# Performance work log

Measured on AMD Instinct MI355X. Metric: run time of the kernel, lower is better.

The kernel has to match this reference:

```python
import jax, jax.numpy as jnp
import numpy as np

B = 2
ROW, COL = 63, 84          # resolution
ROW_, COL_ = 32, 42        # resolution_
N = ROW * COL              # 5292 kv tokens
N_ = ROW_ * COL_           # 1344 q tokens
IN_DIM, OUT_DIM = 256, 512
KEY_DIM, NUM_HEADS, ATTN_RATIO, STRIDE = 16, 8, 2, 2
D = ATTN_RATIO * KEY_DIM   # 32 (value dim per head)
DH = D * NUM_HEADS         # 256
NH_KD = KEY_DIM * NUM_HEADS  # 128
H_KV = DH + NH_KD          # 384
SCALE = KEY_DIM ** -0.5
EPS = 1e-5


def _build_bias_idxs():
    # replicates the itertools.product double loop, vectorized; ids ordered by
    # first occurrence in row-major scan (same as dict insertion order).
    r_ = np.arange(ROW_); c_ = np.arange(COL_)
    r = np.arange(ROW); c = np.arange(COL)
    off_r = np.abs(r_[:, None] * STRIDE - r[None, :])      # (32, 63)
    off_c = np.abs(c_[:, None] * STRIDE - c[None, :])      # (42, 84)
    keys = (off_r[:, None, :, None] * 1000 + off_c[None, :, None, :]).reshape(-1)
    _, first_idx, inv = np.unique(keys, return_index=True, return_inverse=True)
    order = np.argsort(first_idx)
    rank = np.empty_like(order); rank[order] = np.arange(len(order))
    idxs = rank[inv].reshape(N_, N).astype(np.int32)
    return idxs, len(order)


def setup_inputs() -> dict:
    key = jax.random.key(0)
    ks = jax.random.split(key, 12)
    idxs_np, n_off = _build_bias_idxs()
    inp = {
        "x": jax.random.normal(ks[0], (B, N, IN_DIM), jnp.float32),
        "kv_w": jax.random.normal(ks[1], (H_KV, IN_DIM), jnp.float32) * (IN_DIM ** -0.5),
        "kv_g": jnp.ones((H_KV,), jnp.float32),
        "kv_b": jnp.zeros((H_KV,), jnp.float32),
        "q_w": jax.random.normal(ks[2], (NH_KD, IN_DIM), jnp.float32) * (IN_DIM ** -0.5),
        "q_g": jnp.ones((NH_KD,), jnp.float32),
        "q_b": jnp.zeros((NH_KD,), jnp.float32),
        "proj_w": jax.random.normal(ks[3], (OUT_DIM, DH), jnp.float32) * (DH ** -0.5),
        "proj_g": jnp.ones((OUT_DIM,), jnp.float32),
        "proj_b": jnp.zeros((OUT_DIM,), jnp.float32),
        "bias_table": jax.random.normal(ks[4], (NUM_HEADS, n_off), jnp.float32) * 0.02,
        "bias_idxs": jnp.asarray(idxs_np),
    }
    return inp


def _linear_bn(x, w, g, b):
    # Linear (no bias) followed by BatchNorm1d in training mode (batch stats
    # over flattened (B*N) dim, biased variance).
    y = jnp.einsum("bnc,oc->bno", x, w)
    flat = y.reshape(-1, y.shape[-1])
    mu = flat.mean(0)
    var = flat.var(0)
    return (y - mu) * (g / jnp.sqrt(var + EPS)) + b


def _hardswish(x):
    return x * jnp.clip(x + 3.0, 0.0, 6.0) / 6.0


def reference(x, kv_w, kv_g, kv_b, q_w, q_g, q_b, proj_w, proj_g, proj_b,
              bias_table, bias_idxs):
    Bx = x.shape[0]
    # kv projection -> split k (KEY_DIM) and v (D) per head
    kv = _linear_bn(x, kv_w, kv_g, kv_b).reshape(Bx, N, NUM_HEADS, KEY_DIM + D)
    k = kv[..., :KEY_DIM].transpose(0, 2, 1, 3)   # (B, H, N, key_dim)
    v = kv[..., KEY_DIM:].transpose(0, 2, 1, 3)   # (B, H, N, d)
    # q: spatial subsample then projection
    xs = x.reshape(Bx, ROW, COL, IN_DIM)[:, ::STRIDE, ::STRIDE].reshape(Bx, N_, IN_DIM)
    q = _linear_bn(xs, q_w, q_g, q_b).reshape(Bx, N_, NUM_HEADS, KEY_DIM).transpose(0, 2, 1, 3)
    # gathered relative position bias: (H, N_, N)
    ab = bias_table[:, bias_idxs]
    attn = jnp.einsum("bhqd,bhkd->bhqk", q, k) * SCALE + ab[None]
    attn = jax.nn.softmax(attn, axis=-1)
    out = jnp.einsum("bhqk,bhkd->bhqd", attn, v)       # (B, H, N_, d)
    out = out.transpose(0, 2, 1, 3).reshape(Bx, N_, DH)
    out = _linear_bn(_hardswish(out), proj_w, proj_g, proj_b)
    return out
```

## Files before the change

### kernel.cpp

```cpp
#include <hip/hip_runtime.h>
#include <hip/hip_bf16.h>
#include <math.h>

#define N_K 5292
#define N_Q 1344
#define NH_KD 128
#define NROWS 21504
#define LOG2E 1.4426950408889634f
#define MSTAT 16.0f

typedef float f32x4 __attribute__((ext_vector_type(4)));
typedef short short8 __attribute__((ext_vector_type(8)));

__device__ __forceinline__ float fexp2(float x) {
#if __has_builtin(__builtin_amdgcn_exp2f)
    return __builtin_amdgcn_exp2f(x);
#else
    return exp2f(x);
#endif
}

__device__ __forceinline__ unsigned pk_bf16(float a, float b) {
    union { __hip_bfloat162 h; unsigned u; } c;
    c.h = __float22bfloat162_rn(make_float2(a, b));
    return c.u;
}

__device__ __forceinline__ void hilo_pk(float4 v, uint2& hi, uint2& lo) {
    unsigned h0 = pk_bf16(v.x, v.y);
    unsigned h1 = pk_bf16(v.z, v.w);
    float hx = __uint_as_float(h0 << 16);
    float hy = __uint_as_float(h0 & 0xffff0000u);
    float hz = __uint_as_float(h1 << 16);
    float hw = __uint_as_float(h1 & 0xffff0000u);
    hi = make_uint2(h0, h1);
    lo = make_uint2(pk_bf16(v.x - hx, v.y - hy), pk_bf16(v.z - hz, v.w - hw));
}

__global__ __launch_bounds__(256) void prep_kernel(
    const float* __restrict__ x, const float* __restrict__ kv_w,
    const float* __restrict__ q_w, const float* __restrict__ proj_w,
    const float* __restrict__ bias_table, const int* __restrict__ bias_idxs, int n_off,
    float* __restrict__ sums, unsigned short* __restrict__ Xh, unsigned short* __restrict__ Xl,
    unsigned short* __restrict__ Wh, unsigned short* __restrict__ Wl,
    float* __restrict__ bt_r)
{
    int bid = blockIdx.x;
    const int t = threadIdx.x;
    if (bid < 8) {
        int i = bid * 256 + t;
        if (i < 2048) sums[i] = 0.f;
        return;
    }
    bid -= 8;
    if (bid < 2646) {
        int i = bid * 256 + t;
        float4 v = ((const float4*)x)[i];
        uint2 h, l;
        hilo_pk(v, h, l);
        ((uint2*)Xh)[i] = h;
        ((uint2*)Xl)[i] = l;
        return;
    }
    bid -= 2646;
    if (bid < 256) {
        int i = bid * 256 + t;
        int j = i;
        const float* s;
        if (j < 384 * 64) s = kv_w;
        else if ((j -= 384 * 64) < 128 * 64) s = q_w;
        else { j -= 128 * 64; s = proj_w; }
        float4 v = ((const float4*)s)[j];
        uint2 h, l;
        hilo_pk(v, h, l);
        ((uint2*)Wh)[i] = h;
        ((uint2*)Wl)[i] = l;
        return;
    }
    bid -= 256;
    {
        int i = bid * 256 + t;
        if (i < 8 * N_K) {
            int h = i / N_K, j = i - h * N_K;
            bt_r[i] = fmaf(bias_table[h * n_off + bias_idxs[j]], LOG2E, -MSTAT);
        }
    }
}

__device__ __forceinline__ void gemm_core(
    const unsigned short* __restrict__ Ah, const unsigned short* __restrict__ Al,
    const unsigned short* __restrict__ Wh, const unsigned short* __restrict__ Wl,
    float* __restrict__ Y, float* __restrict__ sums,
    int M, int Ncols, int mtiles, int nblk, int mode, int id)
{
    __shared__ unsigned short As_h[64][40], As_l[64][40], Bs_h[64][40], Bs_l[64][40];
    const int xcd = id & 7;
    const int id8 = id >> 3;
    const int my = xcd + (id8 / nblk) * 8;
    const int ny = id8 % nblk;
    if (my >= mtiles) return;

    const int t = threadIdx.x;
    const int w = t >> 6, lane = t & 63, g = lane >> 4, ln = lane & 15;
    const int m0 = my * 64, n0 = ny * 64;
    const int srow = t >> 2;
    const int sc8 = (t & 3) * 8;

    int mrow = m0 + srow;
    long asrc = -1;
    if (mrow < M) {
        if (mode == 1) {
            int bb = mrow / N_Q;
            int i = mrow - bb * N_Q;
            asrc = (long)(bb * N_K + (i / 42) * 168 + (i % 42) * 2);
        } else asrc = mrow;
    }
    const int nrow = n0 + srow;

    f32x4 acc[4];
    #pragma unroll
    for (int nt = 0; nt < 4; ++nt) acc[nt] = (f32x4){0.f, 0.f, 0.f, 0.f};

    for (int k0 = 0; k0 < 256; k0 += 32) {
        uint4 a_h = make_uint4(0, 0, 0, 0), a_l = a_h;
        if (asrc >= 0) {
            a_h = *(const uint4*)(Ah + asrc * 256 + k0 + sc8);
            a_l = *(const uint4*)(Al + asrc * 256 + k0 + sc8);
        }
        uint4 b_h = *(const uint4*)(Wh + (size_t)nrow * 256 + k0 + sc8);
        uint4 b_l = *(const uint4*)(Wl + (size_t)nrow * 256 + k0 + sc8);

        __syncthreads();
        *(uint4*)&As_h[srow][sc8] = a_h;
        *(uint4*)&As_l[srow][sc8] = a_l;
        *(uint4*)&Bs_h[srow][sc8] = b_h;
        *(uint4*)&Bs_l[srow][sc8] = b_l;
        __syncthreads();

        short8 ah = *(const short8*)&As_h[w * 16 + ln][g * 8];
        short8 al = *(const short8*)&As_l[w * 16 + ln][g * 8];
        #pragma unroll
        for (int nt = 0; nt < 4; ++nt) {
            short8 bh = *(const short8*)&Bs_h[nt * 16 + ln][g * 8];
            short8 bl = *(const short8*)&Bs_l[nt * 16 + ln][g * 8];
            acc[nt] = __builtin_amdgcn_mfma_f32_16x16x32_bf16(al, bh, acc[nt], 0, 0, 0);
            acc[nt] = __builtin_amdgcn_mfma_f32_16x16x32_bf16(ah, bl, acc[nt], 0, 0, 0);
            acc[nt] = __builtin_amdgcn_mfma_f32_16x16x32_bf16(ah, bh, acc[nt], 0, 0, 0);
        }
    }

    #pragma unroll
    for (int nt = 0; nt < 4; ++nt) {
        #pragma unroll
        for (int reg = 0; reg < 4; ++reg) {
            int mr = m0 + w * 16 + g * 4 + reg;
            if (mr < M) Y[(size_t)mr * Ncols + n0 + nt * 16 + ln] = acc[nt][reg];
        }
    }

    float s4[4], q4[4];
    #pragma unroll
    for (int nt = 0; nt < 4; ++nt) {
        float s = acc[nt][0] + acc[nt][1] + acc[nt][2] + acc[nt][3];
        float q = fmaf(acc[nt][0], acc[nt][0], fmaf(acc[nt][1], acc[nt][1],
                  fmaf(acc[nt][2], acc[nt][2], acc[nt][3] * acc[nt][3])));
        s += __shfl_xor(s, 16); s += __shfl_xor(s, 32);
        q += __shfl_xor(q, 16); q += __shfl_xor(q, 32);
        s4[nt] = s; q4[nt] = q;
    }
    __syncthreads();
    float* st_s = (float*)&As_h[0][0];
    float* st_q = st_s + 256;
    if (g == 0) {
        #pragma unroll
        for (int nt = 0; nt < 4; ++nt) {
            st_s[(w * 4 + nt) * 16 + ln] = s4[nt];
            st_q[(w * 4 + nt) * 16 + ln] = q4[nt];
        }
    }
    __syncthreads();
    if (t < 64) {
        int nt = t >> 4, c = t & 15;
        float a = 0.f, b2 = 0.f;
        #pragma unroll
        for (int ww = 0; ww < 4; ++ww) {
            a  += st_s[(ww * 4 + nt) * 16 + c];
            b2 += st_q[(ww * 4 + nt) * 16 + c];
        }
        atomicAdd(&sums[n0 + nt * 16 + c], a);
        atomicAdd(&sums[Ncols + n0 + nt * 16 + c], b2);
    }
}

__global__ __launch_bounds__(256) void gemm_qkv(
    const unsigned short* __restrict__ Xh, const unsigned short* __restrict__ Xl,
    const unsigned short* __restrict__ Wh, const unsigned short* __restrict__ Wl,
    float* __restrict__ kv_y, float* __restrict__ q_y,
    float* __restrict__ sums_kv, float* __restrict__ sums_q)
{
    int id = blockIdx.x;
    if (id < 1008)
        gemm_core(Xh, Xl, Wh, Wl, kv_y, sums_kv, 10584, 384, 166, 6, 0, id);
    else
        gemm_core(Xh, Xl, Wh + 384 * 256, Wl + 384 * 256, q_y, sums_q,
                  2688, 128, 42, 2, 1, id - 1008);
}

__global__ __launch_bounds__(256) void gemm_proj(
    const unsigned short* __restrict__ Ah, const unsigned short* __restrict__ Al,
    const unsigned short* __restrict__ Wh, const unsigned short* __restrict__ Wl,
    float* __restrict__ Y, float* __restrict__ sums)
{
    gemm_core(Ah, Al, Wh, Wl, Y, sums, 2688, 512, 42, 8, 0, blockIdx.x);
}

__global__ __launch_bounds__(256) void kv_pack(const float* __restrict__ kv_y,
                                               const float* __restrict__ sums,
                                               const float* __restrict__ kv_g,
                                               const float* __restrict__ kv_b,
                                               unsigned short* __restrict__ Kp,
                                               unsigned short* __restrict__ Vp)
{
    int i = blockIdx.x * 256 + threadIdx.x;
    if (i >= 2 * 8 * N_K * 12) return;
    int c4 = i % 12;
    int key = (i / 12) % N_K;
    int h = (i / (12 * N_K)) & 7;
    int b = i / (12 * N_K * 8);
    int ch = h * 48 + c4 * 4;
    const float inv = 1.f / 10584.f;
    float4 sm = *(const float4*)(sums + ch);
    float4 sq = *(const float4*)(sums + 384 + ch);
    float4 gg = *(const float4*)(kv_g + ch);
    float4 bb = *(const float4*)(kv_b + ch);
    float4 v = *(const float4*)(kv_y + (size_t)(b * N_K + key) * 384 + ch);
    #define BNAPP(c) { float mu = sm.c * inv; \
        float var = fmaf(-mu, mu, sq.c * inv); \
        float s = gg.c * rsqrtf(var + 1e-5f); \
        v.c = fmaf(v.c, s, fmaf(-mu, s, bb.c)); }
    BNAPP(x) BNAPP(y) BNAPP(z) BNAPP(w)
    #undef BNAPP
    uint2 u = make_uint2(pk_bf16(v.x, v.y), pk_bf16(v.z, v.w));
    size_t slot = (size_t)(b * 8 + h) * N_K + key;
    if (c4 < 4) *(uint2*)((unsigned*)Kp + slot * 8 + c4 * 2) = u;
    else        *(uint2*)((unsigned*)Vp + slot * 16 + (c4 - 4) * 2) = u;
}

__global__ __launch_bounds__(256, 5) void attn_mfma(
    const unsigned short* __restrict__ Kp, const unsigned short* __restrict__ Vp,
    const float* __restrict__ q_y, const float* __restrict__ sums,
    const float* __restrict__ q_g, const float* __restrict__ q_b,
    const float* __restrict__ bt_r,
    float* __restrict__ pl, float* __restrict__ pacc)
{
    const int id = blockIdx.x;
    const int h = id & 7;
    const int z = (id >> 3) & 7;
    const int qt = id >> 6;
    const int b = z >> 2, ks = z & 3;
    const int t = threadIdx.x;
    const int w = t >> 6, lane = t & 63, g = lane >> 4, ln = lane & 15;

    __shared__ float bt_s[21 * 84];
    __shared__ unsigned short K_s[2][64][24];
    __shared__ unsigned short Vt_s[2][32][72];
    __shared__ unsigned short P_s[4][16][72];

    const int q0 = qt * 64;
    const int kstart = ks * 1344;
    const int kend = (kstart + 1344 < N_K) ? kstart + 1344 : N_K;
    const int ntiles = (kend - kstart + 63) >> 6;
    const bool tail = (ks == 3);

    const int kr0 = ks * 16;
    const int kr1 = (kend - 1) / 84;
    const int rq2min = (q0 / 42) * 2;
    const int rq2max = ((q0 + 63) / 42) * 2;
    int dr_lo = 0;
    if (rq2min > kr1) dr_lo = rq2min - kr1;
    else if (kr0 > rq2max) dr_lo = kr0 - rq2max;
    int a1 = rq2max - kr0, a2 = kr1 - rq2min;
    int dr_hi = a1 > a2 ? a1 : a2;
    {
        int nb = (dr_hi - dr_lo + 1) * 84;
        const float* src = bt_r + h * N_K + dr_lo * 84;
        for (int j = t; j < nb; j += 256) bt_s[j] = src[j];
    }

    short8 qfrag = (short8)0;
    if (lane < 32) {
        const float inv = 1.f / 2688.f;
        const float post = 0.25f * LOG2E;
        const int c0 = h * 16 + g * 8;
        const float* qp = q_y + (size_t)(b * N_Q + q0 + w * 16 + ln) * NH_KD + c0;
        float vv[8];
        #pragma unroll
        for (int j = 0; j < 8; ++j) {
            float mu  = sums[c0 + j] * inv;
            float var = fmaf(-mu, mu, sums[128 + c0 + j] * inv);
            float s   = q_g[c0 + j] * rsqrtf(var + 1e-5f) * post;
            vv[j] = fmaf(qp[j], s, fmaf(-mu, s, q_b[c0 + j] * post));
        }
        union { short8 s; unsigned u[4]; } qf;
        qf.u[0] = pk_bf16(vv[0], vv[1]); qf.u[1] = pk_bf16(vv[2], vv[3]);
        qf.u[2] = pk_bf16(vv[4], vv[5]); qf.u[3] = pk_bf16(vv[6], vv[7]);
        qfrag = qf.s;
    }

    int rq2[4], cq2[4];
    #pragma unroll
    for (int reg = 0; reg < 4; ++reg) {
        int qg = q0 + w * 16 + g * 4 + reg;
        rq2[reg] = (qg / 42) * 2;
        cq2[reg] = (qg % 42) * 2;
    }
    int kr[4], kc[4];
    #pragma unroll
    for (int st = 0; st < 4; ++st) {
        int kg = kstart + st * 16 + ln;
        kr[st] = kg / 84;
        kc[st] = kg - kr[st] * 84;
    }

    const unsigned* kp_base = (const unsigned*)Kp + (size_t)(b * 8 + h) * N_K * 8;
    const unsigned* vp_base = (const unsigned*)Vp + (size_t)(b * 8 + h) * N_K * 16;
    const int skey = t >> 2, schunk = t & 3;
    const int vslot = ((skey & 15) << 2) | (skey >> 4);
    const int v0 = schunk * 8;

    uint2 kreg; uint4 vreg;
    {
        int kg = kstart + skey; if (kg > N_K - 1) kg = N_K - 1;
        kreg = *(const uint2*)(kp_base + (size_t)kg * 8 + schunk * 2);
        vreg = *(const uint4*)(vp_base + (size_t)kg * 16 + schunk * 4);
    }
    *(uint2*)&K_s[0][skey][schunk * 4] = kreg;
    Vt_s[0][v0 + 0][vslot] = (unsigned short)vreg.x;
    Vt_s[0][v0 + 1][vslot] = (unsigned short)(vreg.x >> 16);
    Vt_s[0][v0 + 2][vslot] = (unsigned short)vreg.y;
    Vt_s[0][v0 + 3][vslot] = (unsigned short)(vreg.y >> 16);
    Vt_s[0][v0 + 4][vslot] = (unsigned short)vreg.z;
    Vt_s[0][v0 + 5][vslot] = (unsigned short)(vreg.z >> 16);
    Vt_s[0][v0 + 6][vslot] = (unsigned short)vreg.w;
    Vt_s[0][v0 + 7][vslot] = (unsigned short)(vreg.w >> 16);
    __syncthreads();

    float l[4] = {0.f, 0.f, 0.f, 0.f};
    f32x4 acc0 = {0.f, 0.f, 0.f, 0.f}, acc1 = {0.f, 0.f, 0.f, 0.f};
    const f32x4 zero4 = {0.f, 0.f, 0.f, 0.f};
    int p = 0;

    for (int it = 0; it < ntiles; ++it) {
        const int k0 = kstart + it * 64;
        const bool notlast = (it + 1 < ntiles);
        if (notlast) {
            int kg = k0 + 64 + skey; if (kg > N_K - 1) kg = N_K - 1;
            kreg = *(const uint2*)(kp_base + (size_t)kg * 8 + schunk * 2);
            vreg = *(const uint4*)(vp_base + (size_t)kg * 16 + schunk * 4);
        }

        f32x4 sf[4];
        #pragma unroll
        for (int st = 0; st < 4; ++st) {
            short8 bf = (short8)0;
            if (lane < 32) bf = *(const short8*)&K_s[p][st * 16 + ln][g * 8];
            sf[st] = __builtin_amdgcn_mfma_f32_16x16x32_bf16(qfrag, bf, zero4, 0, 0, 0);
        }

        float pv[4][4];
        #pragma unroll
        for (int st = 0; st < 4; ++st) {
            #pragma unroll
            for (int reg = 0; reg < 4; ++reg) {
                int dr = rq2[reg] - kr[st]; dr = dr < 0 ? -dr : dr;
                int dc = cq2[reg] - kc[st]; dc = dc < 0 ? -dc : dc;
                pv[st][reg] = fexp2(sf[st][reg] + bt_s[(dr - dr_lo) * 84 + dc]);
            }
        }
        if (tail && it == ntiles - 1) {
            #pragma unroll
            for (int st = 0; st < 4; ++st) {
                bool bad = (k0 + st * 16 + ln) >= N_K;
                #pragma unroll
                for (int reg = 0; reg < 4; ++reg)
                    pv[st][reg] = bad ? 0.f : pv[st][reg];
            }
        }

        #pragma unroll
        for (int reg = 0; reg < 4; ++reg) {
            l[reg] += (pv[0][reg] + pv[1][reg]) + (pv[2][reg] + pv[3][reg]);
            uint2 pw = make_uint2(pk_bf16(pv[0][reg], pv[1][reg]),
                                  pk_bf16(pv[2][reg], pv[3][reg]));
            *(uint2*)&P_s[w][g * 4 + reg][4 * ln] = pw;
        }

        #pragma unroll
        for (int kt = 0; kt < 2; ++kt) {
            short8 af = *(const short8*)&P_s[w][ln][g * 8 + kt * 32];
            short8 b0 = *(const short8*)&Vt_s[p][ln][g * 8 + kt * 32];
            short8 b1 = *(const short8*)&Vt_s[p][ln + 16][g * 8 + kt * 32];
            acc0 = __builtin_amdgcn_mfma_f32_16x16x32_bf16(af, b0, acc0, 0, 0, 0);
            acc1 = __builtin_amdgcn_mfma_f32_16x16x32_bf16(af, b1, acc1, 0, 0, 0);
        }

        if (notlast) {
            int q2 = p ^ 1;
            *(uint2*)&K_s[q2][skey][schunk * 4] = kreg;
            Vt_s[q2][v0 + 0][vslot] = (unsigned short)vreg.x;
            Vt_s[q2][v0 + 1][vslot] = (unsigned short)(vreg.x >> 16);
            Vt_s[q2][v0 + 2][vslot] = (unsigned short)vreg.y;
            Vt_s[q2][v0 + 3][vslot] = (unsigned short)(vreg.y >> 16);
            Vt_s[q2][v0 + 4][vslot] = (unsigned short)vreg.z;
            Vt_s[q2][v0 + 5][vslot] = (unsigned short)(vreg.z >> 16);
            Vt_s[q2][v0 + 6][vslot] = (unsigned short)vreg.w;
            Vt_s[q2][v0 + 7][vslot] = (unsigned short)(vreg.w >> 16);
            __syncthreads();
            p = q2;
        }

        #pragma unroll
        for (int st = 0; st < 4; ++st) {
            kc[st] += 64;
            if (kc[st] >= 84) { kc[st] -= 84; kr[st] += 1; }
        }
    }

    #pragma unroll
    for (int reg = 0; reg < 4; ++reg) {
        float s = l[reg];
        s += __shfl_xor(s, 1, 16);
        s += __shfl_xor(s, 2, 16);
        s += __shfl_xor(s, 4, 16);
        s += __shfl_xor(s, 8, 16);
        l[reg] = s;
    }

    const int rbase = (b * 8 + h) * N_Q + q0 + w * 16;
    #pragma unroll
    for (int reg = 0; reg < 4; ++reg) {
        int prow = ks * NROWS + rbase + g * 4 + reg;
        pacc[(size_t)prow * 32 + ln]      = acc0[reg];
        pacc[(size_t)prow * 32 + 16 + ln] = acc1[reg];
        if (ln == 0) pl[prow] = l[reg];
    }
}

__global__ __launch_bounds__(256) void combine_kernel(const float* __restrict__ pl,
                                                      const float* __restrict__ pacc,
                                                      unsigned short* __restrict__ oh,
                                                      unsigned short* __restrict__ ol)
{
    int i = blockIdx.x * 256 + threadIdx.x;
    int r = i >> 5, e = i & 31;
    float L = (pl[r] + pl[NROWS + r]) + (pl[2 * NROWS + r] + pl[3 * NROWS + r]);
    float v = (pacc[(size_t)r * 32 + e] + pacc[(size_t)(NROWS + r) * 32 + e])
            + (pacc[(size_t)(2 * NROWS + r) * 32 + e] + pacc[(size_t)(3 * NROWS + r) * 32 + e]);
    v /= L;
    float hs = v * fminf(fmaxf(v + 3.f, 0.f), 6.f) * (1.f / 6.f);
    unsigned hu = pk_bf16(hs, 0.f) & 0xffffu;
    float hf = __uint_as_float(hu << 16);
    unsigned lu = pk_bf16(hs - hf, 0.f) & 0xffffu;
    int q = r % N_Q;
    int bh = r / N_Q;
    int hh = bh & 7, b = bh >> 3;
    size_t idx = (size_t)(b * N_Q + q) * 256 + hh * 32 + e;
    oh[idx] = (unsigned short)hu;
    ol[idx] = (unsigned short)lu;
}

__global__ __launch_bounds__(256) void norm_apply(
    const float* __restrict__ Y, const float* __restrict__ sums,
    const float* __restrict__ g, const float* __restrict__ bb,
    float* __restrict__ out, int rows, int cols, float inv_rows)
{
    __shared__ float sc_s[64], sh_s[64];
    const int t = threadIdx.x;
    const int c0 = blockIdx.x * 64;
    if (t < 64) {
        int c = c0 + t;
        float mu  = sums[c] * inv_rows;
        float var = fmaf(-mu, mu, sums[cols + c] * inv_rows);
        float s   = g[c] * rsqrtf(var + 1e-5f);
        sc_s[t] = s;
        sh_s[t] = fmaf(-mu, s, bb[c]);
    }
    __syncthreads();
    const int c4 = (t & 15) * 4;
    float4 scv = *(const float4*)&sc_s[c4];
    float4 shv = *(const float4*)&sh_s[c4];
    for (int r = blockIdx.y * 16 + (t >> 4); r < rows; r += gridDim.y * 16) {
        size_t off = (size_t)r * cols + c0 + c4;
        float4 v = *(const float4*)(Y + off);
        v.x = fmaf(v.x, scv.x, shv.x);
        v.y = fmaf(v.y, scv.y, shv.y);
        v.z = fmaf(v.z, scv.z, shv.z);
        v.w = fmaf(v.w, scv.w, shv.w);
        *(float4*)(out + off) = v;
    }
}

extern "C" void kernel_launch(void* const* d_in, const int* in_sizes, int n_in,
                              void* d_out, int out_size, void* d_ws, size_t ws_size,
                              hipStream_t stream) {
    (void)n_in; (void)out_size; (void)ws_size;
    const float* x      = (const float*)d_in[0];
    const float* kv_w   = (const float*)d_in[1];
    const float* kv_g   = (const float*)d_in[2];
    const float* kv_b   = (const float*)d_in[3];
    const float* q_w    = (const float*)d_in[4];
    const float* q_g    = (const float*)d_in[5];
    const float* q_b    = (const float*)d_in[6];
    const float* proj_w = (const float*)d_in[7];
    const float* proj_g = (const float*)d_in[8];
    const float* proj_b = (const float*)d_in[9];
    const float* bias_table = (const float*)d_in[10];
    const int*   bias_idxs  = (const int*)d_in[11];
    const int    n_off = in_sizes[10] / 8;
    float* out = (float*)d_out;

    float* ws = (float*)d_ws;
    float* kv_y = ws;
    float* q_y  = kv_y + 10584 * 384;
    float* regA = q_y + 2688 * 128;
    unsigned short* Xh = (unsigned short*)regA;
    unsigned short* Xl = Xh + 10584 * 256;
    float* pacc   = regA;
    float* proj_y = regA;
    float* pl = regA + 4 * NROWS * 32;
    unsigned short* Wh = (unsigned short*)(pl + 4 * NROWS);
    unsigned short* Wl = Wh + 1024 * 256;
    unsigned short* attn_oh = Wl + 1024 * 256;
    unsigned short* attn_ol = attn_oh + 2688 * 256;
    unsigned short* Kp = attn_ol + 2688 * 256;
    unsigned short* Vp = Kp + 2 * 8 * N_K * 16;
    float* sums_kv = (float*)(Vp + 2 * 8 * N_K * 32);
    float* sums_q  = sums_kv + 768;
    float* sums_p  = sums_q + 256;
    float* bt_r    = sums_p + 1024;

    prep_kernel<<<3076, 256, 0, stream>>>(x, kv_w, q_w, proj_w, bias_table, bias_idxs,
                                          n_off, sums_kv, Xh, Xl, Wh, Wl, bt_r);
    gemm_qkv<<<1104, 256, 0, stream>>>(Xh, Xl, Wh, Wl, kv_y, q_y, sums_kv, sums_q);
    kv_pack<<<3969, 256, 0, stream>>>(kv_y, sums_kv, kv_g, kv_b, Kp, Vp);
    attn_mfma<<<1344, 256, 0, stream>>>(Kp, Vp, q_y, sums_q, q_g, q_b, bt_r, pl, pacc);
    combine_kernel<<<2688, 256, 0, stream>>>(pl, pacc, attn_oh, attn_ol);
    gemm_proj<<<384, 256, 0, stream>>>(attn_oh, attn_ol, Wh + 512 * 256, Wl + 512 * 256,
                                       proj_y, sums_p);
    norm_apply<<<dim3(8, 84), 256, 0, stream>>>(proj_y, sums_p, proj_g, proj_b, out,
                                                2688, 512, 1.f / 2688.f);
}
```

Measured before the change: 222.1 us.

## Drop split-bf16 GEMM precision and fold kv BatchNorm into attention and combine

The GEMMs now run in plain bf16 instead of the hi/lo three-MFMA split, which cuts MFMA work and operand traffic to a third. The kv GEMM writes raw bf16 K and V directly in the packed per-head layout, so the kv_pack kernel and the fp32 kv_y buffer go away. The kv BatchNorm is applied algebraically instead: the K scale is folded into q, the K shift is dropped because it is constant along each softmax row, and the V affine is applied in combine. This loses precision, since raw K and V are rounded to bf16 before normalisation and no low-order correction is kept, and it may break tolerance.

```diff
diff --git a/kernel.cpp b/kernel.cpp
--- a/kernel.cpp
+++ b/kernel.cpp
@@ -25,25 +25,16 @@
     c.h = __float22bfloat162_rn(make_float2(a, b));
     return c.u;
 }
-
-__device__ __forceinline__ void hilo_pk(float4 v, uint2& hi, uint2& lo) {
-    unsigned h0 = pk_bf16(v.x, v.y);
-    unsigned h1 = pk_bf16(v.z, v.w);
-    float hx = __uint_as_float(h0 << 16);
-    float hy = __uint_as_float(h0 & 0xffff0000u);
-    float hz = __uint_as_float(h1 << 16);
-    float hw = __uint_as_float(h1 & 0xffff0000u);
-    hi = make_uint2(h0, h1);
-    lo = make_uint2(pk_bf16(v.x - hx, v.y - hy), pk_bf16(v.z - hz, v.w - hw));
+__device__ __forceinline__ unsigned short f2bf(float a) {
+    return (unsigned short)pk_bf16(a, 0.f);
 }
 
 __global__ __launch_bounds__(256) void prep_kernel(
     const float* __restrict__ x, const float* __restrict__ kv_w,
     const float* __restrict__ q_w, const float* __restrict__ proj_w,
     const float* __restrict__ bias_table, const int* __restrict__ bias_idxs, int n_off,
-    float* __restrict__ sums, unsigned short* __restrict__ Xh, unsigned short* __restrict__ Xl,
-    unsigned short* __restrict__ Wh, unsigned short* __restrict__ Wl,
-    float* __restrict__ bt_r)
+    float* __restrict__ sums, unsigned short* __restrict__ Xp,
+    unsigned short* __restrict__ Wp, float* __restrict__ bt_r)
 {
     int bid = blockIdx.x;
     const int t = threadIdx.x;
@@ -56,10 +47,7 @@
     if (bid < 2646) {
         int i = bid * 256 + t;
         float4 v = ((const float4*)x)[i];
-        uint2 h, l;
-        hilo_pk(v, h, l);
-        ((uint2*)Xh)[i] = h;
-        ((uint2*)Xl)[i] = l;
+        ((uint2*)Xp)[i] = make_uint2(pk_bf16(v.x, v.y), pk_bf16(v.z, v.w));
         return;
     }
     bid -= 2646;
@@ -71,10 +59,7 @@
         else if ((j -= 384 * 64) < 128 * 64) s = q_w;
         else { j -= 128 * 64; s = proj_w; }
         float4 v = ((const float4*)s)[j];
-        uint2 h, l;
-        hilo_pk(v, h, l);
-        ((uint2*)Wh)[i] = h;
-        ((uint2*)Wl)[i] = l;
+        ((uint2*)Wp)[i] = make_uint2(pk_bf16(v.x, v.y), pk_bf16(v.z, v.w));
         return;
     }
     bid -= 256;
@@ -87,77 +72,40 @@
     }
 }
 
-__device__ __forceinline__ void gemm_core(
-    const unsigned short* __restrict__ Ah, const unsigned short* __restrict__ Al,
-    const unsigned short* __restrict__ Wh, const unsigned short* __restrict__ Wl,
-    float* __restrict__ Y, float* __restrict__ sums,
-    int M, int Ncols, int mtiles, int nblk, int mode, int id)
-{
-    __shared__ unsigned short As_h[64][40], As_l[64][40], Bs_h[64][40], Bs_l[64][40];
-    const int xcd = id & 7;
-    const int id8 = id >> 3;
-    const int my = xcd + (id8 / nblk) * 8;
-    const int ny = id8 % nblk;
-    if (my >= mtiles) return;
-
+__device__ __forceinline__ void gemm_body(
+    const unsigned short* __restrict__ Ap, const unsigned short* __restrict__ Wp,
+    long asrc, int nrow,
+    unsigned short (*As)[40], unsigned short (*Bs)[40], f32x4 acc[4])
+{
     const int t = threadIdx.x;
     const int w = t >> 6, lane = t & 63, g = lane >> 4, ln = lane & 15;
-    const int m0 = my * 64, n0 = ny * 64;
     const int srow = t >> 2;
     const int sc8 = (t & 3) * 8;
 
-    int mrow = m0 + srow;
-    long asrc = -1;
-    if (mrow < M) {
-        if (mode == 1) {
-            int bb = mrow / N_Q;
-            int i = mrow - bb * N_Q;
-            asrc = (long)(bb * N_K + (i / 42) * 168 + (i % 42) * 2);
-        } else asrc = mrow;
-    }
-    const int nrow = n0 + srow;
-
-    f32x4 acc[4];
-    #pragma unroll
-    for (int nt = 0; nt < 4; ++nt) acc[nt] = (f32x4){0.f, 0.f, 0.f, 0.f};
-
     for (int k0 = 0; k0 < 256; k0 += 32) {
-        uint4 a_h = make_uint4(0, 0, 0, 0), a_l = a_h;
-        if (asrc >= 0) {
-            a_h = *(const uint4*)(Ah + asrc * 256 + k0 + sc8);
-            a_l = *(const uint4*)(Al + asrc * 256 + k0 + sc8);
-        }
-        uint4 b_h = *(const uint4*)(Wh + (size_t)nrow * 256 + k0 + sc8);
-        uint4 b_l = *(const uint4*)(Wl + (size_t)nrow * 256 + k0 + sc8);
+        uint4 a = make_uint4(0, 0, 0, 0);
+        if (asrc >= 0) a = *(const uint4*)(Ap + asrc * 256 + k0 + sc8);
+        uint4 b = *(const uint4*)(Wp + (size_t)nrow * 256 + k0 + sc8);
 
         __syncthreads();
-        *(uint4*)&As_h[srow][sc8] = a_h;
-        *(uint4*)&As_l[srow][sc8] = a_l;
-        *(uint4*)&Bs_h[srow][sc8] = b_h;
-        *(uint4*)&Bs_l[srow][sc8] = b_l;
+        *(uint4*)&As[srow][sc8] = a;
+        *(uint4*)&Bs[srow][sc8] = b;
         __syncthreads();
 
-        short8 ah = *(const short8*)&As_h[w * 16 + ln][g * 8];
-        short8 al = *(const short8*)&As_l[w * 16 + ln][g * 8];
+        short8 ah = *(const short8*)&As[w * 16 + ln][g * 8];
         #pragma unroll
         for (int nt = 0; nt < 4; ++nt) {
-            short8 bh = *(const short8*)&Bs_h[nt * 16 + ln][g * 8];
-            short8 bl = *(const short8*)&Bs_l[nt * 16 + ln][g * 8];
-            acc[nt] = __builtin_amdgcn_mfma_f32_16x16x32_bf16(al, bh, acc[nt], 0, 0, 0);
-            acc[nt] = __builtin_amdgcn_mfma_f32_16x16x32_bf16(ah, bl, acc[nt], 0, 0, 0);
+            short8 bh = *(const short8*)&Bs[nt * 16 + ln][g * 8];
             acc[nt] = __builtin_amdgcn_mfma_f32_16x16x32_bf16(ah, bh, acc[nt], 0, 0, 0);
         }
     }
-
-    #pragma unroll
-    for (int nt = 0; nt < 4; ++nt) {
-        #pragma unroll
-        for (int reg = 0; reg < 4; ++reg) {
-            int mr = m0 + w * 16 + g * 4 + reg;
-            if (mr < M) Y[(size_t)mr * Ncols + n0 + nt * 16 + ln] = acc[nt][reg];
-        }
-    }
-
+}
+
+__device__ __forceinline__ void gemm_stats(f32x4 acc[4], float* __restrict__ sums,
+                                           int n0, int Ncols, float* scratch)
+{
+    const int t = threadIdx.x;
+    const int w = t >> 6, lane = t & 63, g = lane >> 4, ln = lane & 15;
     float s4[4], q4[4];
     #pragma unroll
     for (int nt = 0; nt < 4; ++nt) {
@@ -169,8 +117,8 @@
         s4[nt] = s; q4[nt] = q;
     }
     __syncthreads();
-    float* st_s = (float*)&As_h[0][0];
-    float* st_q = st_s + 256;
+    float* st_s = scratch;
+    float* st_q = scratch + 256;
     if (g == 0) {
         #pragma unroll
         for (int nt = 0; nt < 4; ++nt) {
@@ -193,63 +141,106 @@
 }
 
 __global__ __launch_bounds__(256) void gemm_qkv(
-    const unsigned short* __restrict__ Xh, const unsigned short* __restrict__ Xl,
-    const unsigned short* __restrict__ Wh, const unsigned short* __restrict__ Wl,
-    float* __restrict__ kv_y, float* __restrict__ q_y,
-    float* __restrict__ sums_kv, float* __restrict__ sums_q)
-{
+    const unsigned short* __restrict__ Xp, const unsigned short* __restrict__ Wp,
+    unsigned short* __restrict__ Kp, unsigned short* __restrict__ Vp,
+    float* __restrict__ q_y, float* __restrict__ sums_kv, float* __restrict__ sums_q)
+{
+    __shared__ unsigned short As[64][40], Bs[64][40];
+    const int t = threadIdx.x;
+    const int w = t >> 6, lane = t & 63, g = lane >> 4, ln = lane & 15;
+    const int srow = t >> 2;
     int id = blockIdx.x;
-    if (id < 1008)
-        gemm_core(Xh, Xl, Wh, Wl, kv_y, sums_kv, 10584, 384, 166, 6, 0, id);
-    else
-        gemm_core(Xh, Xl, Wh + 384 * 256, Wl + 384 * 256, q_y, sums_q,
-                  2688, 128, 42, 2, 1, id - 1008);
+
+    f32x4 acc[4];
+    #pragma unroll
+    for (int nt = 0; nt < 4; ++nt) acc[nt] = (f32x4){0.f, 0.f, 0.f, 0.f};
+
+    if (id < 1008) {
+        const int xcd = id & 7, id8 = id >> 3;
+        const int my = xcd + (id8 / 6) * 8, ny = id8 % 6;
+        if (my >= 166) return;
+        const int m0 = my * 64, n0 = ny * 64;
+        int mrow = m0 + srow;
+        long asrc = (mrow < 10584) ? mrow : -1;
+        gemm_body(Xp, Wp, asrc, n0 + srow, As, Bs, acc);
+
+        #pragma unroll
+        for (int nt = 0; nt < 4; ++nt) {
+            int c = n0 + nt * 16 + ln;
+            int hh = c / 48, cc = c - 48 * hh;
+            #pragma unroll
+            for (int reg = 0; reg < 4; ++reg) {
+                int mr = m0 + w * 16 + g * 4 + reg;
+                if (mr < 10584) {
+                    int bb = mr >= N_K;
+                    int key = mr - bb * N_K;
+                    unsigned short v16 = f2bf(acc[nt][reg]);
+                    size_t slot = (size_t)(bb * 8 + hh) * N_K + key;
+                    if (cc < 16) Kp[slot * 16 + cc] = v16;
+                    else         Vp[slot * 32 + cc - 16] = v16;
+                }
+            }
+        }
+        gemm_stats(acc, sums_kv, n0, 384, (float*)&As[0][0]);
+    } else {
+        id -= 1008;
+        const int xcd = id & 7, id8 = id >> 3;
+        const int my = xcd + (id8 / 2) * 8, ny = id8 % 2;
+        if (my >= 42) return;
+        const int m0 = my * 64, n0 = ny * 64;
+        int mrow = m0 + srow;
+        long asrc = -1;
+        {
+            int bb = mrow / N_Q;
+            int i = mrow - bb * N_Q;
+            asrc = (long)(bb * N_K + (i / 42) * 168 + (i % 42) * 2);
+        }
+        gemm_body(Xp, Wp + 384 * 256, asrc, n0 + srow, As, Bs, acc);
+
+        #pragma unroll
+        for (int nt = 0; nt < 4; ++nt)
+            #pragma unroll
+            for (int reg = 0; reg < 4; ++reg) {
+                int mr = m0 + w * 16 + g * 4 + reg;
+                q_y[(size_t)mr * 128 + n0 + nt * 16 + ln] = acc[nt][reg];
+            }
+        gemm_stats(acc, sums_q, n0, 128, (float*)&As[0][0]);
+    }
 }
 
 __global__ __launch_bounds__(256) void gemm_proj(
-    const unsigned short* __restrict__ Ah, const unsigned short* __restrict__ Al,
-    const unsigned short* __restrict__ Wh, const unsigned short* __restrict__ Wl,
+    const unsigned short* __restrict__ Ap, const unsigned short* __restrict__ Wp,
     float* __restrict__ Y, float* __restrict__ sums)
 {
-    gemm_core(Ah, Al, Wh, Wl, Y, sums, 2688, 512, 42, 8, 0, blockIdx.x);
-}
-
-__global__ __launch_bounds__(256) void kv_pack(const float* __restrict__ kv_y,
-                                               const float* __restrict__ sums,
-                                               const float* __restrict__ kv_g,
-                                               const float* __restrict__ kv_b,
-                                               unsigned short* __restrict__ Kp,
-                                               unsigned short* __restrict__ Vp)
-{
-    int i = blockIdx.x * 256 + threadIdx.x;
-    if (i >= 2 * 8 * N_K * 12) return;
-    int c4 = i % 12;
-    int key = (i / 12) % N_K;
-    int h = (i / (12 * N_K)) & 7;
-    int b = i / (12 * N_K * 8);
-    int ch = h * 48 + c4 * 4;
-    const float inv = 1.f / 10584.f;
-    float4 sm = *(const float4*)(sums + ch);
-    float4 sq = *(const float4*)(sums + 384 + ch);
-    float4 gg = *(const float4*)(kv_g + ch);
-    float4 bb = *(const float4*)(kv_b + ch);
-    float4 v = *(const float4*)(kv_y + (size_t)(b * N_K + key) * 384 + ch);
-    #define BNAPP(c) { float mu = sm.c * inv; \
-        float var = fmaf(-mu, mu, sq.c * inv); \
-        float s = gg.c * rsqrtf(var + 1e-5f); \
-        v.c = fmaf(v.c, s, fmaf(-mu, s, bb.c)); }
-    BNAPP(x) BNAPP(y) BNAPP(z) BNAPP(w)
-    #undef BNAPP
-    uint2 u = make_uint2(pk_bf16(v.x, v.y), pk_bf16(v.z, v.w));
-    size_t slot = (size_t)(b * 8 + h) * N_K + key;
-    if (c4 < 4) *(uint2*)((unsigned*)Kp + slot * 8 + c4 * 2) = u;
-    else        *(uint2*)((unsigned*)Vp + slot * 16 + (c4 - 4) * 2) = u;
+    __shared__ unsigned short As[64][40], Bs[64][40];
+    const int t = threadIdx.x;
+    const int w = t >> 6, lane = t & 63, g = lane >> 4, ln = lane & 15;
+    const int id = blockIdx.x;
+    const int xcd = id & 7, id8 = id >> 3;
+    const int my = xcd + (id8 / 8) * 8, ny = id8 % 8;
+    if (my >= 42) return;
+    const int m0 = my * 64, n0 = ny * 64;
+
+    f32x4 acc[4];
+    #pragma unroll
+    for (int nt = 0; nt < 4; ++nt) acc[nt] = (f32x4){0.f, 0.f, 0.f, 0.f};
+    gemm_body(Ap, Wp, m0 + (t >> 2), n0 + (t >> 2), As, Bs, acc);
+
+    #pragma unroll
+    for (int nt = 0; nt < 4; ++nt)
+        #pragma unroll
+        for (int reg = 0; reg < 4; ++reg) {
+            int mr = m0 + w * 16 + g * 4 + reg;
+            Y[(size_t)mr * 512 + n0 + nt * 16 + ln] = acc[nt][reg];
+        }
+    gemm_stats(acc, sums, n0, 512, (float*)&As[0][0]);
 }
 
 __global__ __launch_bounds__(256, 5) void attn_mfma(
     const unsigned short* __restrict__ Kp, const unsigned short* __restrict__ Vp,
-    const float* __restrict__ q_y, const float* __restrict__ sums,
+    const float* __restrict__ q_y, const float* __restrict__ sums_q,
     const float* __restrict__ q_g, const float* __restrict__ q_b,
+    const float* __restrict__ sums_kv, const float* __restrict__ kv_g,
     const float* __restrict__ bt_r,
     float* __restrict__ pl, float* __restrict__ pacc)
 {
@@ -289,17 +280,22 @@
 
     short8 qfrag = (short8)0;
     if (lane < 32) {
-        const float inv = 1.f / 2688.f;
+        const float invq = 1.f / 2688.f, invk = 1.f / 10584.f;
         const float post = 0.25f * LOG2E;
         const int c0 = h * 16 + g * 8;
+        const int ck = h * 48 + g * 8;
         const float* qp = q_y + (size_t)(b * N_Q + q0 + w * 16 + ln) * NH_KD + c0;
         float vv[8];
         #pragma unroll
         for (int j = 0; j < 8; ++j) {
-            float mu  = sums[c0 + j] * inv;
-            float var = fmaf(-mu, mu, sums[128 + c0 + j] * inv);
+            float mu  = sums_q[c0 + j] * invq;
+            float var = fmaf(-mu, mu, sums_q[128 + c0 + j] * invq);
             float s   = q_g[c0 + j] * rsqrtf(var + 1e-5f) * post;
-            vv[j] = fmaf(qp[j], s, fmaf(-mu, s, q_b[c0 + j] * post));
+            float vq  = fmaf(qp[j], s, fmaf(-mu, s, q_b[c0 + j] * post));
+            float muk = sums_kv[ck + j] * invk;
+            float vrk = fmaf(-muk, muk, sums_kv[384 + ck + j] * invk);
+            float sk  = kv_g[ck + j] * rsqrtf(vrk + 1e-5f);
+            vv[j] = vq * sk;
         }
         union { short8 s; unsigned u[4]; } qf;
         qf.u[0] = pk_bf16(vv[0], vv[1]); qf.u[1] = pk_bf16(vv[2], vv[3]);
@@ -448,25 +444,28 @@
 
 __global__ __launch_bounds__(256) void combine_kernel(const float* __restrict__ pl,
                                                       const float* __restrict__ pacc,
-                                                      unsigned short* __restrict__ oh,
-                                                      unsigned short* __restrict__ ol)
+                                                      const float* __restrict__ sums_kv,
+                                                      const float* __restrict__ kv_g,
+                                                      const float* __restrict__ kv_b,
+                                                      unsigned short* __restrict__ attn_o)
 {
     int i = blockIdx.x * 256 + threadIdx.x;
     int r = i >> 5, e = i & 31;
     float L = (pl[r] + pl[NROWS + r]) + (pl[2 * NROWS + r] + pl[3 * NROWS + r]);
     float v = (pacc[(size_t)r * 32 + e] + pacc[(size_t)(NROWS + r) * 32 + e])
             + (pacc[(size_t)(2 * NROWS + r) * 32 + e] + pacc[(size_t)(3 * NROWS + r) * 32 + e]);
-    v /= L;
-    float hs = v * fminf(fmaxf(v + 3.f, 0.f), 6.f) * (1.f / 6.f);
-    unsigned hu = pk_bf16(hs, 0.f) & 0xffffu;
-    float hf = __uint_as_float(hu << 16);
-    unsigned lu = pk_bf16(hs - hf, 0.f) & 0xffffu;
     int q = r % N_Q;
     int bh = r / N_Q;
     int hh = bh & 7, b = bh >> 3;
-    size_t idx = (size_t)(b * N_Q + q) * 256 + hh * 32 + e;
-    oh[idx] = (unsigned short)hu;
-    ol[idx] = (unsigned short)lu;
+    const int ch = hh * 48 + 16 + e;
+    const float invk = 1.f / 10584.f;
+    float mu  = sums_kv[ch] * invk;
+    float var = fmaf(-mu, mu, sums_kv[384 + ch] * invk);
+    float s   = kv_g[ch] * rsqrtf(var + 1e-5f);
+    float tt  = fmaf(-mu, s, kv_b[ch]);
+    v = fmaf(s, v / L, tt);
+    float hs = v * fminf(fmaxf(v + 3.f, 0.f), 6.f) * (1.f / 6.f);
+    attn_o[(size_t)(b * N_Q + q) * 256 + hh * 32 + e] = f2bf(hs);
 }
 
 __global__ __launch_bounds__(256) void norm_apply(
@@ -520,19 +519,14 @@
     float* out = (float*)d_out;
 
     float* ws = (float*)d_ws;
-    float* kv_y = ws;
-    float* q_y  = kv_y + 10584 * 384;
-    float* regA = q_y + 2688 * 128;
-    unsigned short* Xh = (unsigned short*)regA;
-    unsigned short* Xl = Xh + 10584 * 256;
-    float* pacc   = regA;
-    float* proj_y = regA;
-    float* pl = regA + 4 * NROWS * 32;
-    unsigned short* Wh = (unsigned short*)(pl + 4 * NROWS);
-    unsigned short* Wl = Wh + 1024 * 256;
-    unsigned short* attn_oh = Wl + 1024 * 256;
-    unsigned short* attn_ol = attn_oh + 2688 * 256;
-    unsigned short* Kp = attn_ol + 2688 * 256;
+    float* q_y  = ws;
+    float* pacc = q_y + 2688 * 128;
+    float* proj_y = pacc;
+    float* pl = pacc + 4 * NROWS * 32;
+    unsigned short* Xp = (unsigned short*)(pl + 4 * NROWS);
+    unsigned short* Wp = Xp + 10584 * 256;
+    unsigned short* attn_o = Wp + 1024 * 256;
+    unsigned short* Kp = attn_o + 2688 * 256;
     unsigned short* Vp = Kp + 2 * 8 * N_K * 16;
     float* sums_kv = (float*)(Vp + 2 * 8 * N_K * 32);
     float* sums_q  = sums_kv + 768;
@@ -540,13 +534,12 @@
     float* bt_r    = sums_p + 1024;
 
     prep_kernel<<<3076, 256, 0, stream>>>(x, kv_w, q_w, proj_w, bias_table, bias_idxs,
-                                          n_off, sums_kv, Xh, Xl, Wh, Wl, bt_r);
-    gemm_qkv<<<1104, 256, 0, stream>>>(Xh, Xl, Wh, Wl, kv_y, q_y, sums_kv, sums_q);
-    kv_pack<<<3969, 256, 0, stream>>>(kv_y, sums_kv, kv_g, kv_b, Kp, Vp);
-    attn_mfma<<<1344, 256, 0, stream>>>(Kp, Vp, q_y, sums_q, q_g, q_b, bt_r, pl, pacc);
-    combine_kernel<<<2688, 256, 0, stream>>>(pl, pacc, attn_oh, attn_ol);
-    gemm_proj<<<384, 256, 0, stream>>>(attn_oh, attn_ol, Wh + 512 * 256, Wl + 512 * 256,
-                                       proj_y, sums_p);
+                                          n_off, sums_kv, Xp, Wp, bt_r);
+    gemm_qkv<<<1104, 256, 0, stream>>>(Xp, Wp, Kp, Vp, q_y, sums_kv, sums_q);
+    attn_mfma<<<1344, 256, 0, stream>>>(Kp, Vp, q_y, sums_q, q_g, q_b,
+                                        sums_kv, kv_g, bt_r, pl, pacc);
+    combine_kernel<<<2688, 256, 0, stream>>>(pl, pacc, sums_kv, kv_g, kv_b, attn_o);
+    gemm_proj<<<8 * 6 * 8, 256, 0, stream>>>(attn_o, Wp + 512 * 256, proj_y, sums_p);
     norm_apply<<<dim3(8, 84), 256, 0, stream>>>(proj_y, sums_p, proj_g, proj_b, out,
                                                 2688, 512, 1.f / 2688.f);
 }
```

Measured after the change: 210.6 us. -5.2%, faster.
